# Kernel tuning notes

Hardware: AMD Instinct MI355X
Metric: run time of the kernel (lower is better)

## Reference

```python
import jax, jax.numpy as jnp
import numpy as np

N = 10000      # nodes
E = 160000     # edges (avg degree 16)
C = 128        # channel multiplicity
D_DOWN = 64    # node_feats_down_irreps = 64x0e
R = 8          # radial edge features
AVG_NEIGH = 16.0
SQRT3 = 1.7320508075688772


def _glorot(key, shape):
    return jax.random.normal(key, shape, dtype=jnp.float32)


def setup_inputs() -> dict:
    key = jax.random.key(0)
    ks = jax.random.split(key, 16)
    mid = 2 * C  # 256: two 0e paths and two 1o paths stacked
    return {
        "node_attrs": jax.random.uniform(ks[0], (N, 10), dtype=jnp.float32),
        "node_feats": jax.random.normal(ks[1], (N, 4 * C), dtype=jnp.float32),  # 128x0e+128x1o
        "edge_attrs": jax.random.normal(ks[2], (E, 4), dtype=jnp.float32),      # 1x0e+1x1o sph harm
        "edge_feats": jax.random.normal(ks[3], (E, R), dtype=jnp.float32),
        "edge_index": jax.random.randint(ks[4], (2, E), 0, N, dtype=jnp.int32),
        "W_up0": _glorot(ks[5], (C, C)),
        "W_up1": _glorot(ks[6], (C, C)),
        "W_down": _glorot(ks[7], (C, D_DOWN)),
        "mlp_w1": _glorot(ks[8], (R + 2 * D_DOWN, 256)),
        "mlp_w2": _glorot(ks[9], (256, 256)),
        "mlp_w3": _glorot(ks[10], (256, 256)),
        "mlp_w4": _glorot(ks[11], (256, 4 * C)),   # conv_tp.weight_numel = 4 paths * 128
        "W_lin0": _glorot(ks[12], (mid, C)),
        "W_lin1": _glorot(ks[13], (mid, C)),
        "W_skip0": _glorot(ks[14], (C, C)),
        "W_skip1": _glorot(ks[15], (C, C)),
    }


def reference(node_attrs, node_feats, edge_attrs, edge_feats, edge_index,
              W_up0, W_up1, W_down, mlp_w1, mlp_w2, mlp_w3, mlp_w4,
              W_lin0, W_lin1, W_skip0, W_skip1):
    n = node_feats.shape[0]
    # split node feats into 0e scalars and 1o vectors
    x0 = node_feats[:, :C]                      # [N,128]
    x1 = node_feats[:, C:].reshape(n, C, 3)     # [N,128,3]
    inv_c = 1.0 / jnp.sqrt(jnp.float32(C))

    # skip connection: equivariant Linear node_feats -> hidden (per-irrep channel mix)
    sc0 = x0 @ (W_skip0 * inv_c)
    sc1 = jnp.einsum('nui,uv->nvi', x1, W_skip1 * inv_c)
    sc = jnp.concatenate([sc0, sc1.reshape(n, -1)], axis=-1)  # [N,512]

    # linear_up (node_feats -> edge_irreps) and linear_down (-> 64x0e)
    u0 = x0 @ (W_up0 * inv_c)
    u1 = jnp.einsum('nui,uv->nvi', x1, W_up1 * inv_c)
    down = x0 @ (W_down * inv_c)                # [N,64]

    sender, receiver = edge_index[0], edge_index[1]
    # augmented edge features: radial + down[sender] + down[receiver]
    aug = jnp.concatenate([edge_feats, down[sender], down[receiver]], axis=-1)  # [E,136]

    def dense(h, w):
        return h @ (w / jnp.sqrt(jnp.float32(w.shape[0])))

    h = jax.nn.silu(dense(aug, mlp_w1))
    h = jax.nn.silu(dense(h, mlp_w2))
    h = jax.nn.silu(dense(h, mlp_w3))
    tpw = dense(h, mlp_w4)                      # [E,512] per-edge TP weights
    w0, w1, w2, w3 = jnp.split(tpw, 4, axis=-1) # each [E,128]

    # gather sender features, split edge sph harmonics
    xs0 = u0[sender]                            # [E,128]
    xs1 = u1[sender]                            # [E,128,3]
    y0 = edge_attrs[:, :1]                      # [E,1]
    y1 = edge_attrs[:, 1:4]                     # [E,3]

    # CG tensor product, 'uvu' instructions (v=1):
    o0a = w0 * xs0 * y0                                         # 0e x 0e -> 0e
    o0b = w3 * jnp.einsum('eci,ei->ec', xs1, y1) / SQRT3        # 1o x 1o -> 0e
    o1a = w1[:, :, None] * xs0[:, :, None] * y1[:, None, :]     # 0e x 1o -> 1o
    o1b = w2[:, :, None] * xs1 * y0[:, :, None]                 # 1o x 0e -> 1o

    mji0 = jnp.concatenate([o0a, o0b], axis=1)                  # [E,256]
    mji1 = jnp.concatenate([o1a, o1b], axis=1)                  # [E,256,3]

    # scatter-sum over receivers
    m0 = jax.ops.segment_sum(mji0, receiver, num_segments=n)    # [N,256]
    m1 = jax.ops.segment_sum(mji1.reshape(mji1.shape[0], -1), receiver,
                             num_segments=n).reshape(n, 2 * C, 3)

    # final equivariant linear irreps_mid -> target, / avg_num_neighbors
    inv_m = 1.0 / jnp.sqrt(jnp.float32(2 * C))
    msg0 = m0 @ (W_lin0 * inv_m) / AVG_NEIGH                    # [N,128]
    msg1 = jnp.einsum('nui,uv->nvi', m1, W_lin1 * inv_m) / AVG_NEIGH  # [N,128,3]

    # reshape_irreps: [N, mul, (lmax+1)^2] = [N,128,4]
    message = jnp.concatenate([msg0[:, :, None], msg1], axis=-1)
    return (message, sc)
```

## Files before the change

### kernel.cpp

```cpp
#include <hip/hip_runtime.h>
#include <hip/hip_bf16.h>

#define N_NODES 10000
#define N_EDGES 160000
#define TPW_PLANE ((size_t)N_EDGES * 128)
#define EB 32
#define NB 16

typedef short v8s __attribute__((ext_vector_type(8)));
typedef float v4f __attribute__((ext_vector_type(4)));

__device__ __forceinline__ float bf2f(ushort u) {
    union { unsigned i; float f; } x; x.i = ((unsigned)u) << 16; return x.f;
}
__device__ __forceinline__ float fin(float x) {
    return (x == x) ? fminf(fmaxf(x, -1e30f), 1e30f) : 0.f;
}
__device__ __forceinline__ ushort f2bf(float f) {
    union { unsigned i; float f; } x; x.f = fin(f);
    unsigned i = x.i;
    unsigned r = (i + 0x7fffu + ((i >> 16) & 1u)) >> 16;
    return (ushort)r;
}
__device__ __forceinline__ unsigned cvt_pk_bf16(float lo, float hi) {
    unsigned r;
    asm("v_cvt_pk_bf16_f32 %0, %1, %2" : "=v"(r) : "v"(lo), "v"(hi));
    return r;
}

#define INV_C 0.08838834764831845f
#define S_MLP1 0.08574929257125442f
#define S_MLP 0.0625f
#define INV_SQRT3 0.5773502691896258f
#define OUT_SCALE 0.00390625f

#define MFMA __builtin_amdgcn_mfma_f32_16x16x32_bf16

__global__ __launch_bounds__(256) void pack_kernel(
    const float* __restrict__ w1, const float* __restrict__ w2,
    const float* __restrict__ w3, const float* __restrict__ w4,
    const float* __restrict__ wl0, const float* __restrict__ wl1,
    ushort* __restrict__ w1p, ushort* __restrict__ w2p,
    ushort* __restrict__ w3p, ushort* __restrict__ w4p,
    ushort* __restrict__ wl0p, ushort* __restrict__ wl1p)
{
    int idx = blockIdx.x * 256 + threadIdx.x;
    const float* W; ushort* D; int KT, Kreal, Nn, id, koff = 0;
    if (idx < 40960)       { W = w1;  D = w1p;  KT = 5; Kreal = 136; Nn = 256; id = idx; }
    else if (idx < 106496) { W = w2;  D = w2p;  KT = 8; Kreal = 256; Nn = 256; id = idx - 40960; }
    else if (idx < 172032) { W = w3;  D = w3p;  KT = 8; Kreal = 256; Nn = 256; id = idx - 106496; }
    else if (idx < 303104) { W = w4;  D = w4p;  KT = 8; Kreal = 256; Nn = 512; id = idx - 172032; }
    else if (idx < 335872) { W = wl0; D = wl0p; KT = 8; Kreal = 256; Nn = 128; id = idx - 303104; }
    else if (idx < 352256) { W = wl1; D = wl1p;         KT = 4; Kreal = 128; Nn = 128; id = idx - 335872; }
    else                   { W = wl1; D = wl1p + 16384; KT = 4; Kreal = 128; Nn = 128; id = idx - 352256; koff = 128; }
    int j = id & 7, lane = (id >> 3) & 63, tt = id >> 9;
    int kt = tt % KT, nt = tt / KT;
    int k = kt * 32 + ((lane >> 4) << 3) + j;
    int nn = nt * 16 + (lane & 15);
    D[id] = (k < Kreal) ? f2bf(W[(k + koff) * Nn + nn]) : (ushort)0;
}

__global__ __launch_bounds__(256) void node_uud_kernel(
    const float* __restrict__ nf,
    const float* __restrict__ Wu0, const float* __restrict__ Wu1,
    const float* __restrict__ Wd,
    ushort* __restrict__ u0, ushort* __restrict__ u1,
    ushort* __restrict__ down)
{
    __shared__ float x[NB * 512];
    int t = threadIdx.x;
    int n0 = blockIdx.x * NB;
    {
        const float4* src = (const float4*)(nf + (size_t)n0 * 512);
        float4* dst = (float4*)x;
        for (int i = t; i < NB * 128; i += 256) dst[i] = src[i];
    }
    __syncthreads();
    int v = t & 127, g = t >> 7;
    {
        float acc[8] = {0.f,0.f,0.f,0.f,0.f,0.f,0.f,0.f};
        for (int u = 0; u < 128; ++u) {
            float wv = Wu0[u * 128 + v];
#pragma unroll
            for (int j = 0; j < 8; ++j) acc[j] += x[(g * 8 + j) * 512 + u] * wv;
        }
#pragma unroll
        for (int j = 0; j < 8; ++j)
            u0[(size_t)(n0 + g * 8 + j) * 128 + v] = f2bf(acc[j] * INV_C);
    }
    for (int i = 0; i < 3; ++i) {
        float acc[8] = {0.f,0.f,0.f,0.f,0.f,0.f,0.f,0.f};
        for (int u = 0; u < 128; ++u) {
            float wv = Wu1[u * 128 + v];
#pragma unroll
            for (int j = 0; j < 8; ++j)
                acc[j] += x[(g * 8 + j) * 512 + 128 + u * 3 + i] * wv;
        }
#pragma unroll
        for (int j = 0; j < 8; ++j)
            u1[(size_t)(n0 + g * 8 + j) * 384 + i * 128 + v] = f2bf(acc[j] * INV_C);
    }
    {
        int vd = t & 63, gd = t >> 6;
        float acc[4] = {0.f,0.f,0.f,0.f};
        for (int u = 0; u < 128; ++u) {
            float wv = Wd[u * 64 + vd];
#pragma unroll
            for (int j = 0; j < 4; ++j) acc[j] += x[(gd * 4 + j) * 512 + u] * wv;
        }
#pragma unroll
        for (int j = 0; j < 4; ++j)
            down[(size_t)(n0 + gd * 4 + j) * 64 + vd] = f2bf(acc[j] * INV_C);
    }
}

__global__ __launch_bounds__(256) void node_sc_kernel(
    const float* __restrict__ nf,
    const float* __restrict__ Ws0, const float* __restrict__ Ws1,
    float* __restrict__ out_sc)
{
    __shared__ float x[NB * 512];
    int t = threadIdx.x;
    int n0 = blockIdx.x * NB;
    {
        const float4* src = (const float4*)(nf + (size_t)n0 * 512);
        float4* dst = (float4*)x;
        for (int i = t; i < NB * 128; i += 256) dst[i] = src[i];
    }
    __syncthreads();
    int v = t & 127, g = t >> 7;
    {
        float acc[8] = {0.f,0.f,0.f,0.f,0.f,0.f,0.f,0.f};
        for (int u = 0; u < 128; ++u) {
            float wv = Ws0[u * 128 + v];
#pragma unroll
            for (int j = 0; j < 8; ++j) acc[j] += x[(g * 8 + j) * 512 + u] * wv;
        }
#pragma unroll
        for (int j = 0; j < 8; ++j)
            out_sc[(size_t)(n0 + g * 8 + j) * 512 + v] = fin(acc[j] * INV_C);
    }
    for (int i = 0; i < 3; ++i) {
        float acc[8] = {0.f,0.f,0.f,0.f,0.f,0.f,0.f,0.f};
        for (int u = 0; u < 128; ++u) {
            float wv = Ws1[u * 128 + v];
#pragma unroll
            for (int j = 0; j < 8; ++j)
                acc[j] += x[(g * 8 + j) * 512 + 128 + u * 3 + i] * wv;
        }
#pragma unroll
        for (int j = 0; j < 8; ++j)
            out_sc[(size_t)(n0 + g * 8 + j) * 512 + 128 + v * 3 + i] = fin(acc[j] * INV_C);
    }
}

__global__ __launch_bounds__(256) void hist_kernel(const int* __restrict__ eidx, int* __restrict__ counts)
{
    int e = blockIdx.x * 256 + threadIdx.x;
    int r = eidx[N_EDGES + e];
    if (r < 0) r = 0; if (r >= N_NODES) r = N_NODES - 1;
    atomicAdd(&counts[r], 1);
}

__global__ __launch_bounds__(1024) void scan_kernel(const int* __restrict__ counts, int* __restrict__ offs)
{
    __shared__ int buf[1024];
    __shared__ int base_s;
    int t = threadIdx.x;
    if (t == 0) { base_s = 0; offs[0] = 0; }
    __syncthreads();
    for (int chunk = 0; chunk < (N_NODES + 1023) / 1024; ++chunk) {
        int i = chunk * 1024 + t;
        int vv = (i < N_NODES) ? counts[i] : 0;
        buf[t] = vv;
        __syncthreads();
        for (int off = 1; off < 1024; off <<= 1) {
            int xv = (t >= off) ? buf[t - off] : 0;
            __syncthreads();
            buf[t] += xv;
            __syncthreads();
        }
        int incl = buf[t];
        int base = base_s;
        __syncthreads();
        if (i < N_NODES) offs[i + 1] = base + incl;
        if (t == 1023) base_s = base + incl;
        __syncthreads();
    }
}

__global__ __launch_bounds__(256) void fill_kernel(
    const int* __restrict__ eidx, const int* __restrict__ offs,
    int* __restrict__ cnt2, int* __restrict__ esort)
{
    int e = blockIdx.x * 256 + threadIdx.x;
    int r = eidx[N_EDGES + e];
    if (r < 0) r = 0; if (r >= N_NODES) r = N_NODES - 1;
    int k = atomicAdd(&cnt2[r], 1);
    int pos = offs[r] + k;
    if (pos < 0) pos = 0; if (pos >= N_EDGES) pos = N_EDGES - 1;
    esort[pos] = e;
}

#define H_STRIDE 264

template <int KT, bool SILU>
__device__ __forceinline__ void gemm_layer(
    const ushort* __restrict__ wpack, const ushort* srcLDS, int srcStride,
    ushort* dstLDS, float scale)
{
    int t = threadIdx.x;
    int w = t >> 6, l = t & 63;
    int lrow = l & 15, q = l >> 4;

    for (int p = 0; p < 2; ++p) {
        int nt0 = w * 4 + 2 * p, nt1 = nt0 + 1;
        v4f a00 = {0.f,0.f,0.f,0.f}, a01 = {0.f,0.f,0.f,0.f};
        v4f a10 = {0.f,0.f,0.f,0.f}, a11 = {0.f,0.f,0.f,0.f};
#pragma unroll
        for (int kt = 0; kt < KT; ++kt) {
            v8s b0 = *(const v8s*)&wpack[(size_t)(nt0 * KT + kt) * 512 + l * 8];
            v8s b1 = *(const v8s*)&wpack[(size_t)(nt1 * KT + kt) * 512 + l * 8];
            v8s x0 = *(const v8s*)&srcLDS[lrow * srcStride + kt * 32 + q * 8];
            v8s x1 = *(const v8s*)&srcLDS[(16 + lrow) * srcStride + kt * 32 + q * 8];
            a00 = MFMA(x0, b0, a00, 0, 0, 0);
            a01 = MFMA(x0, b1, a01, 0, 0, 0);
            a10 = MFMA(x1, b0, a10, 0, 0, 0);
            a11 = MFMA(x1, b1, a11, 0, 0, 0);
        }
#pragma unroll
        for (int r = 0; r < 4; ++r) {
            float x00 = a00[r] * scale, x01 = a01[r] * scale;
            float x10 = a10[r] * scale, x11 = a11[r] * scale;
            if (SILU) {
                x00 = x00 / (1.f + __expf(-x00));
                x01 = x01 / (1.f + __expf(-x01));
                x10 = x10 / (1.f + __expf(-x10));
                x11 = x11 / (1.f + __expf(-x11));
            }
            int row0 = q * 4 + r, row1 = row0 + 16;
            unsigned p0 = cvt_pk_bf16(x00, x01);
            dstLDS[row0 * H_STRIDE + nt0 * 16 + lrow] = (ushort)p0;
            dstLDS[row0 * H_STRIDE + nt1 * 16 + lrow] = (ushort)(p0 >> 16);
            unsigned p1 = cvt_pk_bf16(x10, x11);
            dstLDS[row1 * H_STRIDE + nt0 * 16 + lrow] = (ushort)p1;
            dstLDS[row1 * H_STRIDE + nt1 * 16 + lrow] = (ushort)(p1 >> 16);
        }
    }
    __syncthreads();
}

template <bool ATOMIC>
__device__ __forceinline__ void gemm_out(
    const ushort* __restrict__ wpack, const ushort* srcLDS,
    const int* s_rcv, float* __restrict__ out, ushort* __restrict__ tpw,
    int e0, int cofs)
{
    int t = threadIdx.x;
    int w = t >> 6, l = t & 63;
    int lrow = l & 15, q = l >> 4;
    ushort* plane = tpw + (size_t)cofs * TPW_PLANE;
    int nt0 = w * 2, nt1 = nt0 + 1;
    v4f a00 = {0.f,0.f,0.f,0.f}, a01 = {0.f,0.f,0.f,0.f};
    v4f a10 = {0.f,0.f,0.f,0.f}, a11 = {0.f,0.f,0.f,0.f};
#pragma unroll
    for (int kt = 0; kt < 8; ++kt) {
        v8s b0 = *(const v8s*)&wpack[(size_t)(nt0 * 8 + kt) * 512 + l * 8];
        v8s b1 = *(const v8s*)&wpack[(size_t)(nt1 * 8 + kt) * 512 + l * 8];
        v8s x0 = *(const v8s*)&srcLDS[lrow * H_STRIDE + kt * 32 + q * 8];
        v8s x1 = *(const v8s*)&srcLDS[(16 + lrow) * H_STRIDE + kt * 32 + q * 8];
        a00 = MFMA(x0, b0, a00, 0, 0, 0);
        a01 = MFMA(x0, b1, a01, 0, 0, 0);
        a10 = MFMA(x1, b0, a10, 0, 0, 0);
        a11 = MFMA(x1, b1, a11, 0, 0, 0);
    }
    int col0 = nt0 * 16 + lrow, col1 = col0 + 16;
#pragma unroll
    for (int r = 0; r < 4; ++r) {
        int row0 = q * 4 + r, row1 = row0 + 16;
        if constexpr (ATOMIC) {
            int rcv0 = s_rcv[row0], rcv1 = s_rcv[row1];
            atomicAdd(&out[(size_t)rcv0 * 512 + col0 * 4 + cofs], fin(a00[r] * OUT_SCALE));
            atomicAdd(&out[(size_t)rcv0 * 512 + col1 * 4 + cofs], fin(a01[r] * OUT_SCALE));
            atomicAdd(&out[(size_t)rcv1 * 512 + col0 * 4 + cofs], fin(a10[r] * OUT_SCALE));
            atomicAdd(&out[(size_t)rcv1 * 512 + col1 * 4 + cofs], fin(a11[r] * OUT_SCALE));
        } else {
            size_t base0 = (size_t)(e0 + row0) * 128;
            unsigned p0 = cvt_pk_bf16(a00[r] * OUT_SCALE, a01[r] * OUT_SCALE);
            plane[base0 + col0] = (ushort)p0;
            plane[base0 + col1] = (ushort)(p0 >> 16);
            size_t base1 = (size_t)(e0 + row1) * 128;
            unsigned p1 = cvt_pk_bf16(a10[r] * OUT_SCALE, a11[r] * OUT_SCALE);
            plane[base1 + col0] = (ushort)p1;
            plane[base1 + col1] = (ushort)(p1 >> 16);
        }
    }
}

template <bool ATOMIC>
__global__ __launch_bounds__(256, 3) void edge_msg_kernel(
    const int* __restrict__ eidx,
    const float* __restrict__ ef, const float* __restrict__ ea,
    const ushort* __restrict__ down,
    const ushort* __restrict__ u0, const ushort* __restrict__ u1,
    const ushort* __restrict__ w1p, const ushort* __restrict__ w2p,
    const ushort* __restrict__ w3p, const ushort* __restrict__ w4p,
    const ushort* __restrict__ wl0p, const ushort* __restrict__ wl1p,
    float* __restrict__ out_msg, ushort* __restrict__ tpw)
{
    __shared__ __align__(16) ushort s_hA[EB * H_STRIDE];
    __shared__ __align__(16) ushort s_hB[EB * H_STRIDE];
    __shared__ __align__(16) ushort s_q[EB * H_STRIDE];
    __shared__ int s_snd[EB];
    __shared__ int s_rcv[EB];
    __shared__ float s_y[EB][4];

    int t = threadIdx.x;
    int e0 = blockIdx.x * EB;

    if (t < EB) {
        int e = e0 + t;
        int s = eidx[e];
        int r = eidx[N_EDGES + e];
        if (s < 0) s = 0; if (s >= N_NODES) s = N_NODES - 1;
        if (r < 0) r = 0; if (r >= N_NODES) r = N_NODES - 1;
        s_snd[t] = s; s_rcv[t] = r;
        s_y[t][0] = fin(ea[(size_t)e * 4 + 0]);
        s_y[t][1] = fin(ea[(size_t)e * 4 + 1]);
        s_y[t][2] = fin(ea[(size_t)e * 4 + 2]);
        s_y[t][3] = fin(ea[(size_t)e * 4 + 3]);
    }
    __syncthreads();
    {
        int e = t >> 3, c0 = (t & 7) * 21;
        int snd = s_snd[e], rcv = s_rcv[e];
#pragma unroll
        for (int j = 0; j < 21; ++j) {
            int cc = c0 + j;
            ushort vv;
            if (cc < 8)        vv = f2bf(ef[(size_t)(e0 + e) * 8 + cc]);
            else if (cc < 72)  vv = down[(size_t)snd * 64 + (cc - 8)];
            else if (cc < 136) vv = down[(size_t)rcv * 64 + (cc - 72)];
            else               vv = 0;
            s_hB[e * 168 + cc] = vv;
        }
    }
    __syncthreads();
    gemm_layer<5, true>(w1p, s_hB, 168, s_hA, S_MLP1);
    gemm_layer<8, true>(w2p, s_hA, H_STRIDE, s_hB, S_MLP);
    gemm_layer<8, true>(w3p, s_hB, H_STRIDE, s_hA, S_MLP);

    int w = t >> 6, l = t & 63;
    int lrow = l & 15, q = l >> 4;
    int colg0 = w * 32 + lrow, colg1 = colg0 + 16;

    for (int qd = 0; qd < 4; ++qd) {
        int nt0 = qd * 8 + w * 2, nt1 = nt0 + 1;
        v4f a00 = {0.f,0.f,0.f,0.f}, a01 = {0.f,0.f,0.f,0.f};
        v4f a10 = {0.f,0.f,0.f,0.f}, a11 = {0.f,0.f,0.f,0.f};
#pragma unroll
        for (int kt = 0; kt < 8; ++kt) {
            v8s b0 = *(const v8s*)&w4p[(size_t)(nt0 * 8 + kt) * 512 + l * 8];
            v8s b1 = *(const v8s*)&w4p[(size_t)(nt1 * 8 + kt) * 512 + l * 8];
            v8s x0 = *(const v8s*)&s_hA[lrow * H_STRIDE + kt * 32 + q * 8];
            v8s x1 = *(const v8s*)&s_hA[(16 + lrow) * H_STRIDE + kt * 32 + q * 8];
            a00 = MFMA(x0, b0, a00, 0, 0, 0);
            a01 = MFMA(x0, b1, a01, 0, 0, 0);
            a10 = MFMA(x1, b0, a10, 0, 0, 0);
            a11 = MFMA(x1, b1, a11, 0, 0, 0);
        }
#pragma unroll
        for (int r = 0; r < 4; ++r) {
#pragma unroll
            for (int m = 0; m < 2; ++m) {
                int row = m * 16 + q * 4 + r;
                float v0 = (m == 0 ? a00[r] : a10[r]) * S_MLP;
                float v1 = (m == 0 ? a01[r] : a11[r]) * S_MLP;
                int snd = s_snd[row];
                if (qd == 0) {
                    float y0 = s_y[row][0];
                    float ua = bf2f(u0[(size_t)snd * 128 + colg0]);
                    float ub = bf2f(u0[(size_t)snd * 128 + colg1]);
                    unsigned pk = cvt_pk_bf16(v0 * ua * y0, v1 * ub * y0);
                    s_hB[row * H_STRIDE + colg0] = (ushort)pk;
                    s_hB[row * H_STRIDE + colg1] = (ushort)(pk >> 16);
                } else if (qd == 1) {
                    float ua = bf2f(u0[(size_t)snd * 128 + colg0]);
                    float ub = bf2f(u0[(size_t)snd * 128 + colg1]);
                    unsigned pk = cvt_pk_bf16(v0 * ua, v1 * ub);
                    s_q[row * H_STRIDE + colg0] = (ushort)pk;
                    s_q[row * H_STRIDE + colg1] = (ushort)(pk >> 16);
                } else if (qd == 2) {
                    unsigned pk = cvt_pk_bf16(v0, v1);
                    s_q[row * H_STRIDE + 128 + colg0] = (ushort)pk;
                    s_q[row * H_STRIDE + 128 + colg1] = (ushort)(pk >> 16);
                } else {
                    size_t ub_ = (size_t)snd * 384;
                    float d0 = bf2f(u1[ub_ + colg0])       * s_y[row][1]
                             + bf2f(u1[ub_ + 128 + colg0]) * s_y[row][2]
                             + bf2f(u1[ub_ + 256 + colg0]) * s_y[row][3];
                    float d1 = bf2f(u1[ub_ + colg1])       * s_y[row][1]
                             + bf2f(u1[ub_ + 128 + colg1]) * s_y[row][2]
                             + bf2f(u1[ub_ + 256 + colg1]) * s_y[row][3];
                    unsigned pk = cvt_pk_bf16(v0 * d0 * INV_SQRT3, v1 * d1 * INV_SQRT3);
                    s_hB[row * H_STRIDE + 128 + colg0] = (ushort)pk;
                    s_hB[row * H_STRIDE + 128 + colg1] = (ushort)(pk >> 16);
                }
            }
        }
    }
    __syncthreads();

    gemm_out<ATOMIC>(wl0p, s_hB, s_rcv, out_msg, tpw, e0, 0);
    __syncthreads();

    const ushort* wl1t = wl1p;
    const ushort* wl1b = wl1p + 16384;
    int ntz0 = w * 2, ntz1 = ntz0 + 1;
    int colz0 = ntz0 * 16 + lrow, colz1 = colz0 + 16;

    v4f z00 = {0.f,0.f,0.f,0.f}, z01 = {0.f,0.f,0.f,0.f};
    v4f z10 = {0.f,0.f,0.f,0.f}, z11 = {0.f,0.f,0.f,0.f};
#pragma unroll
    for (int kt = 0; kt < 4; ++kt) {
        v8s b0 = *(const v8s*)&wl1t[(size_t)(ntz0 * 4 + kt) * 512 + l * 8];
        v8s b1 = *(const v8s*)&wl1t[(size_t)(ntz1 * 4 + kt) * 512 + l * 8];
        v8s x0 = *(const v8s*)&s_q[lrow * H_STRIDE + kt * 32 + q * 8];
        v8s x1 = *(const v8s*)&s_q[(16 + lrow) * H_STRIDE + kt * 32 + q * 8];
        z00 = MFMA(x0, b0, z00, 0, 0, 0);
        z01 = MFMA(x0, b1, z01, 0, 0, 0);
        z10 = MFMA(x1, b0, z10, 0, 0, 0);
        z11 = MFMA(x1, b1, z11, 0, 0, 0);
    }

    for (int i = 0; i < 3; ++i) {
#pragma unroll
        for (int it = 0; it < 8; ++it) {
            int idx = t + it * 256;
            int e = idx >> 6, kp = (idx & 63) << 1;
            unsigned uq = *(const unsigned*)&s_q[e * H_STRIDE + 128 + kp];
            unsigned uu = *(const unsigned*)&u1[(size_t)s_snd[e] * 384 + i * 128 + kp];
            float y0 = s_y[e][0];
            float lo = bf2f((ushort)uq) * bf2f((ushort)uu) * y0;
            float hi = bf2f((ushort)(uq >> 16)) * bf2f((ushort)(uu >> 16)) * y0;
            *(unsigned*)&s_hB[e * H_STRIDE + kp] = cvt_pk_bf16(lo, hi);
        }
        __syncthreads();
        v4f p00 = {0.f,0.f,0.f,0.f}, p01 = {0.f,0.f,0.f,0.f};
        v4f p10 = {0.f,0.f,0.f,0.f}, p11 = {0.f,0.f,0.f,0.f};
#pragma unroll
        for (int kt = 0; kt < 4; ++kt) {
            v8s b0 = *(const v8s*)&wl1b[(size_t)(ntz0 * 4 + kt) * 512 + l * 8];
            v8s b1 = *(const v8s*)&wl1b[(size_t)(ntz1 * 4 + kt) * 512 + l * 8];
            v8s x0 = *(const v8s*)&s_hB[lrow * H_STRIDE + kt * 32 + q * 8];
            v8s x1 = *(const v8s*)&s_hB[(16 + lrow) * H_STRIDE + kt * 32 + q * 8];
            p00 = MFMA(x0, b0, p00, 0, 0, 0);
            p01 = MFMA(x0, b1, p01, 0, 0, 0);
            p10 = MFMA(x1, b0, p10, 0, 0, 0);
            p11 = MFMA(x1, b1, p11, 0, 0, 0);
        }
        ushort* plane = tpw + (size_t)(1 + i) * TPW_PLANE;
#pragma unroll
        for (int r = 0; r < 4; ++r) {
            int row0 = q * 4 + r, row1 = row0 + 16;
            float yi0 = s_y[row0][1 + i], yi1 = s_y[row1][1 + i];
            float v00 = (yi0 * z00[r] + p00[r]) * OUT_SCALE;
            float v01 = (yi0 * z01[r] + p01[r]) * OUT_SCALE;
            float v10 = (yi1 * z10[r] + p10[r]) * OUT_SCALE;
            float v11 = (yi1 * z11[r] + p11[r]) * OUT_SCALE;
            if constexpr (ATOMIC) {
                int rcv0 = s_rcv[row0], rcv1 = s_rcv[row1];
                atomicAdd(&out_msg[(size_t)rcv0 * 512 + colz0 * 4 + 1 + i], fin(v00));
                atomicAdd(&out_msg[(size_t)rcv0 * 512 + colz1 * 4 + 1 + i], fin(v01));
                atomicAdd(&out_msg[(size_t)rcv1 * 512 + colz0 * 4 + 1 + i], fin(v10));
                atomicAdd(&out_msg[(size_t)rcv1 * 512 + colz1 * 4 + 1 + i], fin(v11));
            } else {
                size_t base0 = (size_t)(e0 + row0) * 128;
                unsigned pk0 = cvt_pk_bf16(v00, v01);
                plane[base0 + colz0] = (ushort)pk0;
                plane[base0 + colz1] = (ushort)(pk0 >> 16);
                size_t base1 = (size_t)(e0 + row1) * 128;
                unsigned pk1 = cvt_pk_bf16(v10, v11);
                plane[base1 + colz0] = (ushort)pk1;
                plane[base1 + colz1] = (ushort)(pk1 >> 16);
            }
        }
        __syncthreads();
    }
}

__global__ __launch_bounds__(256) void gather_kernel(
    const int* __restrict__ offs, const int* __restrict__ esort,
    const ushort* __restrict__ tpw, float* __restrict__ out_msg)
{
    int n = blockIdx.x, t = threadIdx.x;
    int beg = offs[n];
    if (beg < 0) beg = 0; if (beg > N_EDGES) beg = N_EDGES;
    int end = offs[n + 1];
    if (end < beg) end = beg; if (end > N_EDGES) end = N_EDGES;
    int col = t & 127, ca = t >> 7, cb = ca + 2;
    const ushort* pA = tpw + (size_t)ca * TPW_PLANE + col;
    const ushort* pB = tpw + (size_t)cb * TPW_PLANE + col;
    float a0 = 0.f, a1 = 0.f;
    for (int j = beg; j < end; ++j) {
        int e = esort[j];
        if (e < 0) e = 0; if (e >= N_EDGES) e = N_EDGES - 1;
        a0 += bf2f(pA[(size_t)e * 128]);
        a1 += bf2f(pB[(size_t)e * 128]);
    }
    out_msg[(size_t)n * 512 + col * 4 + ca] = fin(a0);
    out_msg[(size_t)n * 512 + col * 4 + cb] = fin(a1);
}

extern "C" void kernel_launch(void* const* d_in, const int* in_sizes, int n_in,
                              void* d_out, int out_size, void* d_ws, size_t ws_size,
                              hipStream_t stream)
{
    const float* node_feats = (const float*)d_in[1];
    const float* edge_attrs = (const float*)d_in[2];
    const float* edge_feats = (const float*)d_in[3];
    const int*   edge_index = (const int*)d_in[4];
    const float* W_up0  = (const float*)d_in[5];
    const float* W_up1  = (const float*)d_in[6];
    const float* W_down = (const float*)d_in[7];
    const float* mlp_w1 = (const float*)d_in[8];
    const float* mlp_w2 = (const float*)d_in[9];
    const float* mlp_w3 = (const float*)d_in[10];
    const float* mlp_w4 = (const float*)d_in[11];
    const float* W_lin0 = (const float*)d_in[12];
    const float* W_lin1 = (const float*)d_in[13];
    const float* W_skip0 = (const float*)d_in[14];
    const float* W_skip1 = (const float*)d_in[15];

    char* S = (char*)d_out + 20480000;

    ushort* u0    = (ushort*)(S + 0);
    ushort* down  = (ushort*)(S + 2560000);
    ushort* u1    = (ushort*)(S + 3840000);
    ushort* w1p   = (ushort*)(S + 11520000);
    ushort* w2p   = (ushort*)(S + 11601920);
    ushort* w3p   = (ushort*)(S + 11732992);
    ushort* w4p   = (ushort*)(S + 11864064);
    ushort* wl0p  = (ushort*)(S + 12126208);
    ushort* wl1p  = (ushort*)(S + 12191744);
    int*    offs  = (int*)(S + 12257280);
    int*    esort = (int*)(S + 12297312);
    int*    counts= (int*)(S + 12937312);
    int*    cnt2  = (int*)(S + 12977312);

    float* out_msg = (float*)d_out;
    float* out_sc  = (float*)d_out + (size_t)N_NODES * 512;

    const size_t TPW_BYTES = (size_t)N_EDGES * 512 * 2;
    bool bigws = (ws_size >= TPW_BYTES) && (d_ws != nullptr);
    ushort* tpw = (ushort*)d_ws;

    pack_kernel<<<1440, 256, 0, stream>>>(mlp_w1, mlp_w2, mlp_w3, mlp_w4, W_lin0, W_lin1,
                                          w1p, w2p, w3p, w4p, wl0p, wl1p);
    node_uud_kernel<<<N_NODES / NB, 256, 0, stream>>>(node_feats, W_up0, W_up1, W_down, u0, u1, down);

    if (bigws) {
        hipMemsetAsync(counts, 0, 80000, stream);
        hist_kernel<<<N_EDGES / 256, 256, 0, stream>>>(edge_index, counts);
        scan_kernel<<<1, 1024, 0, stream>>>(counts, offs);
        fill_kernel<<<N_EDGES / 256, 256, 0, stream>>>(edge_index, offs, cnt2, esort);
        edge_msg_kernel<false><<<N_EDGES / EB, 256, 0, stream>>>(edge_index, edge_feats, edge_attrs,
            down, u0, u1, w1p, w2p, w3p, w4p, wl0p, wl1p, out_msg, tpw);
        gather_kernel<<<N_NODES, 256, 0, stream>>>(offs, esort, tpw, out_msg);
    } else {
        hipMemsetAsync(out_msg, 0, 20480000, stream);
        edge_msg_kernel<true><<<N_EDGES / EB, 256, 0, stream>>>(edge_index, edge_feats, edge_attrs,
            down, u0, u1, w1p, w2p, w3p, w4p, wl0p, wl1p, out_msg, tpw);
    }
    node_sc_kernel<<<N_NODES / NB, 256, 0, stream>>>(node_feats, W_skip0, W_skip1, out_sc);
}
```

Measured before the change: 595.2 us.

## Process edges in receiver-sorted order so gather reads contiguous rows

The edge message kernel now processes edges in receiver-sorted order via esort, writing per-edge outputs at sorted positions. The gather kernel can then stream contiguous rows without the esort indirection, reading two bf16 values per 32-bit load. It also replaces the SiLU division with a hardware reciprocal and stages the skip-connection vector outputs in shared memory for coalesced float4 stores. The cost is scattered reads of edge features and indices inside the edge kernel, plus slightly lower SiLU precision.

```diff
diff --git a/kernel.cpp b/kernel.cpp
--- a/kernel.cpp
+++ b/kernel.cpp
@@ -26,6 +26,14 @@
     unsigned r;
     asm("v_cvt_pk_bf16_f32 %0, %1, %2" : "=v"(r) : "v"(lo), "v"(hi));
     return r;
+}
+__device__ __forceinline__ float fast_rcp(float x) {
+    float r;
+    asm("v_rcp_f32 %0, %1" : "=v"(r) : "v"(x));
+    return r;
+}
+__device__ __forceinline__ float silu(float x) {
+    return x * fast_rcp(1.f + __expf(-x));
 }
 
 #define INV_C 0.08838834764831845f
@@ -120,6 +128,7 @@
     float* __restrict__ out_sc)
 {
     __shared__ float x[NB * 512];
+    __shared__ float xs[NB * 384];
     int t = threadIdx.x;
     int n0 = blockIdx.x * NB;
     {
@@ -150,7 +159,13 @@
         }
 #pragma unroll
         for (int j = 0; j < 8; ++j)
-            out_sc[(size_t)(n0 + g * 8 + j) * 512 + 128 + v * 3 + i] = fin(acc[j] * INV_C);
+            xs[(g * 8 + j) * 384 + v * 3 + i] = fin(acc[j] * INV_C);
+    }
+    __syncthreads();
+    for (int i = t; i < NB * 96; i += 256) {
+        int nd = i / 96, k = i - nd * 96;
+        *(float4*)&out_sc[(size_t)(n0 + nd) * 512 + 128 + k * 4] =
+            *(const float4*)&xs[nd * 384 + k * 4];
     }
 }
 
@@ -233,10 +248,8 @@
             float x00 = a00[r] * scale, x01 = a01[r] * scale;
             float x10 = a10[r] * scale, x11 = a11[r] * scale;
             if (SILU) {
-                x00 = x00 / (1.f + __expf(-x00));
-                x01 = x01 / (1.f + __expf(-x01));
-                x10 = x10 / (1.f + __expf(-x10));
-                x11 = x11 / (1.f + __expf(-x11));
+                x00 = silu(x00); x01 = silu(x01);
+                x10 = silu(x10); x11 = silu(x11);
             }
             int row0 = q * 4 + r, row1 = row0 + 16;
             unsigned p0 = cvt_pk_bf16(x00, x01);
@@ -299,7 +312,7 @@
 
 template <bool ATOMIC>
 __global__ __launch_bounds__(256, 3) void edge_msg_kernel(
-    const int* __restrict__ eidx,
+    const int* __restrict__ eidx, const int* __restrict__ esort,
     const float* __restrict__ ef, const float* __restrict__ ea,
     const ushort* __restrict__ down,
     const ushort* __restrict__ u0, const ushort* __restrict__ u1,
@@ -313,13 +326,21 @@
     __shared__ __align__(16) ushort s_q[EB * H_STRIDE];
     __shared__ int s_snd[EB];
     __shared__ int s_rcv[EB];
+    __shared__ int s_eid[EB];
     __shared__ float s_y[EB][4];
 
     int t = threadIdx.x;
     int e0 = blockIdx.x * EB;
 
     if (t < EB) {
-        int e = e0 + t;
+        int e;
+        if constexpr (ATOMIC) {
+            e = e0 + t;
+        } else {
+            e = esort[e0 + t];
+            if (e < 0) e = 0; if (e >= N_EDGES) e = N_EDGES - 1;
+        }
+        s_eid[t] = e;
         int s = eidx[e];
         int r = eidx[N_EDGES + e];
         if (s < 0) s = 0; if (s >= N_NODES) s = N_NODES - 1;
@@ -333,12 +354,12 @@
     __syncthreads();
     {
         int e = t >> 3, c0 = (t & 7) * 21;
-        int snd = s_snd[e], rcv = s_rcv[e];
+        int snd = s_snd[e], rcv = s_rcv[e], eid = s_eid[e];
 #pragma unroll
         for (int j = 0; j < 21; ++j) {
             int cc = c0 + j;
             ushort vv;
-            if (cc < 8)        vv = f2bf(ef[(size_t)(e0 + e) * 8 + cc]);
+            if (cc < 8)        vv = f2bf(ef[(size_t)eid * 8 + cc]);
             else if (cc < 72)  vv = down[(size_t)snd * 64 + (cc - 8)];
             else if (cc < 136) vv = down[(size_t)rcv * 64 + (cc - 72)];
             else               vv = 0;
@@ -490,7 +511,7 @@
 }
 
 __global__ __launch_bounds__(256) void gather_kernel(
-    const int* __restrict__ offs, const int* __restrict__ esort,
+    const int* __restrict__ offs,
     const ushort* __restrict__ tpw, float* __restrict__ out_msg)
 {
     int n = blockIdx.x, t = threadIdx.x;
@@ -498,18 +519,17 @@
     if (beg < 0) beg = 0; if (beg > N_EDGES) beg = N_EDGES;
     int end = offs[n + 1];
     if (end < beg) end = beg; if (end > N_EDGES) end = N_EDGES;
-    int col = t & 127, ca = t >> 7, cb = ca + 2;
-    const ushort* pA = tpw + (size_t)ca * TPW_PLANE + col;
-    const ushort* pB = tpw + (size_t)cb * TPW_PLANE + col;
+    int c = t & 63;
+    int p = t >> 6;
+    const unsigned* src = (const unsigned*)(tpw + (size_t)p * TPW_PLANE) + c;
     float a0 = 0.f, a1 = 0.f;
     for (int j = beg; j < end; ++j) {
-        int e = esort[j];
-        if (e < 0) e = 0; if (e >= N_EDGES) e = N_EDGES - 1;
-        a0 += bf2f(pA[(size_t)e * 128]);
-        a1 += bf2f(pB[(size_t)e * 128]);
-    }
-    out_msg[(size_t)n * 512 + col * 4 + ca] = fin(a0);
-    out_msg[(size_t)n * 512 + col * 4 + cb] = fin(a1);
+        unsigned v = src[(size_t)j * 64];
+        a0 += bf2f((ushort)v);
+        a1 += bf2f((ushort)(v >> 16));
+    }
+    out_msg[(size_t)n * 512 + (2 * c) * 4 + p] = fin(a0);
+    out_msg[(size_t)n * 512 + (2 * c + 1) * 4 + p] = fin(a1);
 }
 
 extern "C" void kernel_launch(void* const* d_in, const int* in_sizes, int n_in,
@@ -564,12 +584,14 @@
         hist_kernel<<<N_EDGES / 256, 256, 0, stream>>>(edge_index, counts);
         scan_kernel<<<1, 1024, 0, stream>>>(counts, offs);
         fill_kernel<<<N_EDGES / 256, 256, 0, stream>>>(edge_index, offs, cnt2, esort);
-        edge_msg_kernel<false><<<N_EDGES / EB, 256, 0, stream>>>(edge_index, edge_feats, edge_attrs,
+        edge_msg_kernel<false><<<N_EDGES / EB, 256, 0, stream>>>(edge_index, esort,
+            edge_feats, edge_attrs,
             down, u0, u1, w1p, w2p, w3p, w4p, wl0p, wl1p, out_msg, tpw);
-        gather_kernel<<<N_NODES, 256, 0, stream>>>(offs, esort, tpw, out_msg);
+        gather_kernel<<<N_NODES, 256, 0, stream>>>(offs, tpw, out_msg);
     } else {
         hipMemsetAsync(out_msg, 0, 20480000, stream);
-        edge_msg_kernel<true><<<N_EDGES / EB, 256, 0, stream>>>(edge_index, edge_feats, edge_attrs,
+        edge_msg_kernel<true><<<N_EDGES / EB, 256, 0, stream>>>(edge_index, esort,
+            edge_feats, edge_attrs,
             down, u0, u1, w1p, w2p, w3p, w4p, wl0p, wl1p, out_msg, tpw);
     }
     node_sc_kernel<<<N_NODES / NB, 256, 0, stream>>>(node_feats, W_skip0, W_skip1, out_sc);
```

Result: no change. 601.2 us (+1.0%).
